# Kernel optimization log

Measured on AMD Instinct MI355X. Metric: run time of the kernel, lower is better.

## Reference

```python
import jax, jax.numpy as jnp
import numpy as np

D_MODEL = 1024
HEAD_DIM = 128
NUM_HEADS = 8


def setup_inputs() -> dict:
    key = jax.random.key(0)
    ks = jax.random.split(key, 7)
    s = 0.02
    x = jax.random.normal(ks[0], (1, 4096, D_MODEL), dtype=jnp.float32)
    Wq = jax.random.normal(ks[1], (D_MODEL, NUM_HEADS * HEAD_DIM), dtype=jnp.float32) * s
    bq = jnp.zeros((NUM_HEADS * HEAD_DIM,), dtype=jnp.float32)
    Wk = jax.random.normal(ks[2], (D_MODEL, HEAD_DIM), dtype=jnp.float32) * s
    bk = jnp.zeros((HEAD_DIM,), dtype=jnp.float32)
    Wv = jax.random.normal(ks[3], (D_MODEL, HEAD_DIM), dtype=jnp.float32) * s
    bv = jnp.zeros((HEAD_DIM,), dtype=jnp.float32)
    return {"x": x, "Wq": Wq, "bq": bq, "Wk": Wk, "bk": bk, "Wv": Wv, "bv": bv}


def reference(x, Wq, bq, Wk, bk, Wv, bv):
    b, s, _ = x.shape
    q = (x @ Wq + bq).reshape(b, s, NUM_HEADS, HEAD_DIM)  # [b,s,h,d]
    k = x @ Wk + bk  # [b,s,d] shared across heads
    v = x @ Wv + bv  # [b,s,d]
    scale = 1.0 / jnp.sqrt(jnp.float32(HEAD_DIM))
    # scores: [b,h,q,k]
    scores = jnp.einsum('bqhd,bkd->bhqk', q, k) * scale
    attn = jax.nn.softmax(scores, axis=-1)
    out = jnp.einsum('bhqk,bkd->bqhd', attn, v)  # [b,s,h,d]
    return out.reshape(b, s, NUM_HEADS * HEAD_DIM)
```

## Files before the change

### kernel.cpp

```cpp
#include <hip/hip_runtime.h>
#include <hip/hip_bf16.h>
#include <stdint.h>

#define D_MODEL 1024
#define HEAD_DIM 128
#define NUM_HEADS 8
#define SEQ 4096
#define NQKV 1280

using bf16x8 = __attribute__((ext_vector_type(8))) short;
using f32x4  = __attribute__((ext_vector_type(4))) float;

__device__ __forceinline__ unsigned short f32_to_bf16(float f) {
    union { float f; uint32_t u; } c{f};
    uint32_t u = c.u;
    return (unsigned short)((u + 0x7fffu + ((u >> 16) & 1u)) >> 16);
}
__device__ __forceinline__ unsigned int pack_bf16x2(float lo, float hi) {
    return (unsigned int)f32_to_bf16(lo) | ((unsigned int)f32_to_bf16(hi) << 16);
}

__device__ __forceinline__ void dma16(const void* g, void* l) {
    __builtin_amdgcn_global_load_lds(
        (const __attribute__((address_space(1))) unsigned int*)g,
        (__attribute__((address_space(3))) unsigned int*)l, 16, 0, 0);
}

__global__ void cvt_x(const float4* __restrict__ x, int4* __restrict__ xb, int n8) {
    int i = blockIdx.x * blockDim.x + threadIdx.x;
    if (i >= n8) return;
    float4 a = x[2 * i], b = x[2 * i + 1];
    int4 o;
    o.x = (int)pack_bf16x2(a.x, a.y);
    o.y = (int)pack_bf16x2(a.z, a.w);
    o.z = (int)pack_bf16x2(b.x, b.y);
    o.w = (int)pack_bf16x2(b.z, b.w);
    xb[i] = o;
}

__global__ __launch_bounds__(256) void pack_wt(const float* __restrict__ Wq,
                                               const float* __restrict__ Wk,
                                               const float* __restrict__ Wv,
                                               unsigned short* __restrict__ Wt) {
    __shared__ unsigned short tile[64][72];
    int bt = blockIdx.x;
    int ktile = bt & 15, ntile = bt >> 4;
    int k0 = ktile * 64, n0 = ntile * 64;
    const float* W; int ldw, nc0;
    if (n0 < 1024)      { W = Wq; ldw = 1024; nc0 = n0; }
    else if (n0 < 1152) { W = Wk; ldw = 128;  nc0 = n0 - 1024; }
    else                { W = Wv; ldw = 128;  nc0 = n0 - 1152; }
    int t = threadIdx.x;
    int c = t & 63, r0 = t >> 6;
#pragma unroll
    for (int p = 0; p < 16; ++p) {
        int r = r0 + p * 4;
        tile[c][r] = f32_to_bf16(W[(k0 + r) * ldw + nc0 + c]);
    }
    __syncthreads();
#pragma unroll
    for (int p = 0; p < 16; ++p) {
        int rn = r0 + p * 4;
        Wt[(n0 + rn) * 1024 + k0 + c] = tile[rn][c];
    }
}

__global__ __launch_bounds__(256, 3) void qkv_gemm(
    const unsigned short* __restrict__ xb,
    const unsigned short* __restrict__ Wt,
    const float* __restrict__ bq, const float* __restrict__ bk, const float* __restrict__ bv,
    unsigned short* __restrict__ q_bf,
    unsigned short* __restrict__ k_bf,
    unsigned short* __restrict__ v_tmp)
{
    __shared__ unsigned short As[2][128 * 64];
    __shared__ unsigned short Bs[2][64 * 64];
    const int t = threadIdx.x;
    const int lane = t & 63, wave = t >> 6;
    const int l15 = lane & 15, quad = lane >> 4;
    const int m0 = blockIdx.y * 128, n0 = blockIdx.x * 64;
    const int srow_l = lane >> 3;
    const int sc_phys = lane & 7;

    f32x4 acc[2][4];
#pragma unroll
    for (int i = 0; i < 2; ++i)
#pragma unroll
        for (int j = 0; j < 4; ++j) acc[i][j] = (f32x4)0.0f;

    auto issue = [&](int k0c, int buf) {
        int c = sc_phys ^ srow_l;
#pragma unroll
        for (int p = 0; p < 4; ++p) {
            int rb = (wave * 4 + p) * 8;
            dma16(&xb[(m0 + rb + srow_l) * 1024 + k0c + c * 8], &As[buf][rb * 64]);
        }
#pragma unroll
        for (int p = 0; p < 2; ++p) {
            int rb = (wave * 2 + p) * 8;
            dma16(&Wt[(n0 + rb + srow_l) * 1024 + k0c + c * 8], &Bs[buf][rb * 64]);
        }
    };

    issue(0, 0);
    for (int kst = 0; kst < 16; ++kst) {
        const int buf = kst & 1;
        __syncthreads();
        if (kst < 15) issue((kst + 1) * 64, buf ^ 1);
#pragma unroll
        for (int ks = 0; ks < 2; ++ks) {
            bf16x8 a[2], b[4];
#pragma unroll
            for (int mt = 0; mt < 2; ++mt)
                a[mt] = *(const bf16x8*)&As[buf][(wave * 32 + mt * 16 + l15) * 64 + (((ks * 4 + quad) ^ (l15 & 7)) * 8)];
#pragma unroll
            for (int nt = 0; nt < 4; ++nt)
                b[nt] = *(const bf16x8*)&Bs[buf][(nt * 16 + l15) * 64 + (((ks * 4 + quad) ^ (l15 & 7)) * 8)];
#pragma unroll
            for (int mt = 0; mt < 2; ++mt)
#pragma unroll
                for (int nt = 0; nt < 4; ++nt)
                    acc[mt][nt] = __builtin_amdgcn_mfma_f32_16x16x32_bf16(a[mt], b[nt], acc[mt][nt], 0, 0, 0);
        }
    }

    const float qscale = 0.08838834764831843f * 1.4426950408889634f;
#pragma unroll
    for (int mt = 0; mt < 2; ++mt)
#pragma unroll
        for (int nt = 0; nt < 4; ++nt)
#pragma unroll
            for (int r = 0; r < 4; ++r) {
                int row = m0 + wave * 32 + mt * 16 + quad * 4 + r;
                int col = n0 + nt * 16 + l15;
                float v = acc[mt][nt][r];
                if (col < 1024)
                    q_bf[row * 1024 + col] = f32_to_bf16((v + bq[col]) * qscale);
                else if (col < 1152)
                    k_bf[row * 128 + (col - 1024)] = f32_to_bf16(v + bk[col - 1024]);
                else
                    v_tmp[row * 128 + (col - 1152)] = f32_to_bf16(v + bv[col - 1152]);
            }
}

__global__ __launch_bounds__(256) void transpose_v(const unsigned short* __restrict__ v_tmp,
                                                   unsigned short* __restrict__ vt) {
    __shared__ unsigned short tile[64][72];
    int s0 = blockIdx.x * 64, d0 = blockIdx.y * 64;
    int t = threadIdx.x;
    int c = t & 63, r0 = t >> 6;
#pragma unroll
    for (int p = 0; p < 16; ++p) {
        int r = r0 + p * 4;
        tile[c][r] = v_tmp[(s0 + r) * 128 + d0 + c];
    }
    __syncthreads();
#pragma unroll
    for (int p = 0; p < 16; ++p) {
        int rd = r0 + p * 4;
        vt[(d0 + rd) * 4096 + s0 + c] = tile[rd][c];
    }
}

__global__ __launch_bounds__(512, 2) void mqa_attn(
    const unsigned short* __restrict__ q_bf,
    const unsigned short* __restrict__ k_bf,
    const unsigned short* __restrict__ vt_bf,
    float* __restrict__ out)
{
    __shared__ unsigned short Ks[2][2][64 * 128];
    __shared__ unsigned short Vs[2][128 * 64];
    __shared__ unsigned short Ps[8][2][16 * 72];
    const int t = threadIdx.x;
    const int lane = t & 63, wave = t >> 6;
    const int l15 = lane & 15, quad = lane >> 4;
    const int half = wave >> 2, w2 = wave & 3;
    const int qbase = blockIdx.x * 32 + (w2 & 1) * 16;
    const int h0 = blockIdx.y * 4 + (w2 >> 1) * 2;
    const int kbase = half * 2048;

    const int krow_l = lane >> 4;
    const int kc_phys = lane & 15;
    const int vrow_l = lane >> 3;
    const int vc_phys = lane & 7;

    bf16x8 qf[2][4];
    {
        int qrow = qbase + l15;
#pragma unroll
        for (int g = 0; g < 2; ++g)
#pragma unroll
            for (int ks = 0; ks < 4; ++ks)
                qf[g][ks] = *(const bf16x8*)&q_bf[qrow * 1024 + (h0 + g) * 128 + ks * 32 + quad * 8];
    }

    f32x4 o[2][8];
#pragma unroll
    for (int g = 0; g < 2; ++g)
#pragma unroll
        for (int d = 0; d < 8; ++d) o[g][d] = (f32x4)0.0f;
    float l_part[2][4] = {{0.f, 0.f, 0.f, 0.f}, {0.f, 0.f, 0.f, 0.f}};

    auto issueK = [&](int kt, int buf) {
#pragma unroll
        for (int p = 0; p < 4; ++p) {
            int row = w2 * 16 + p * 4 + krow_l;
            int c = kc_phys ^ (row & 15);
            dma16(&k_bf[(kt + row) * 128 + c * 8], &Ks[half][buf][(w2 * 16 + p * 4) * 128]);
        }
    };
    auto issueV = [&](int kt) {
#pragma unroll
        for (int p = 0; p < 4; ++p) {
            int row = w2 * 32 + p * 8 + vrow_l;
            int c = vc_phys ^ vrow_l;
            dma16(&vt_bf[row * 4096 + kt + c * 8], &Vs[half][(w2 * 32 + p * 8) * 64]);
        }
    };

    issueK(kbase, 0);
    for (int it = 0; it < 32; ++it) {
        const int buf = it & 1;
        __syncthreads();
        issueV(kbase + it * 64);
        const bool pk = (it + 1 < 32);
        if (pk) issueK(kbase + (it + 1) * 64, buf ^ 1);

        f32x4 s[2][4];
#pragma unroll
        for (int g = 0; g < 2; ++g)
#pragma unroll
            for (int nt = 0; nt < 4; ++nt) s[g][nt] = (f32x4)0.0f;
#pragma unroll
        for (int ks = 0; ks < 4; ++ks)
#pragma unroll
            for (int nt = 0; nt < 4; ++nt) {
                int row = nt * 16 + l15;
                bf16x8 kb = *(const bf16x8*)&Ks[half][buf][row * 128 + (((ks * 4 + quad) ^ l15) * 8)];
                s[0][nt] = __builtin_amdgcn_mfma_f32_16x16x32_bf16(qf[0][ks], kb, s[0][nt], 0, 0, 0);
                s[1][nt] = __builtin_amdgcn_mfma_f32_16x16x32_bf16(qf[1][ks], kb, s[1][nt], 0, 0, 0);
            }

#pragma unroll
        for (int g = 0; g < 2; ++g) {
            unsigned short* P = &Ps[wave][g][0];
#pragma unroll
            for (int nt = 0; nt < 4; ++nt)
#pragma unroll
                for (int r = 0; r < 4; ++r) {
                    float pv = __builtin_amdgcn_exp2f(s[g][nt][r]);
                    l_part[g][r] += pv;
                    P[(quad * 4 + r) * 72 + nt * 16 + l15] = f32_to_bf16(pv);
                }
        }
        asm volatile("s_waitcnt lgkmcnt(0)" ::: "memory");
        if (pk) asm volatile("s_waitcnt vmcnt(4)" ::: "memory");
        else    asm volatile("s_waitcnt vmcnt(0)" ::: "memory");

#pragma unroll
        for (int ks = 0; ks < 2; ++ks) {
            bf16x8 pa0 = *(const bf16x8*)&Ps[wave][0][l15 * 72 + ks * 32 + quad * 8];
            bf16x8 pa1 = *(const bf16x8*)&Ps[wave][1][l15 * 72 + ks * 32 + quad * 8];
#pragma unroll
            for (int d = 0; d < 8; ++d) {
                int row = d * 16 + l15;
                bf16x8 vb = *(const bf16x8*)&Vs[half][row * 64 + (((ks * 4 + quad) ^ (l15 & 7)) * 8)];
                o[0][d] = __builtin_amdgcn_mfma_f32_16x16x32_bf16(pa0, vb, o[0][d], 0, 0, 0);
                o[1][d] = __builtin_amdgcn_mfma_f32_16x16x32_bf16(pa1, vb, o[1][d], 0, 0, 0);
            }
        }
    }

#pragma unroll
    for (int g = 0; g < 2; ++g)
#pragma unroll
        for (int r = 0; r < 4; ++r) {
#pragma unroll
            for (int off = 1; off < 16; off <<= 1)
                l_part[g][r] += __shfl_xor(l_part[g][r], off, 64);
        }

    __syncthreads();
    float* Xo = (float*)&Ks[0][0][0];
    float* Xl = (float*)&Vs[0][0];
    if (half == 1) {
#pragma unroll
        for (int g = 0; g < 2; ++g)
#pragma unroll
            for (int d = 0; d < 8; ++d)
                *(f32x4*)&Xo[((w2 * 16 + g * 8 + d) * 64 + lane) * 4] = o[g][d];
#pragma unroll
        for (int g = 0; g < 2; ++g)
#pragma unroll
            for (int r = 0; r < 4; ++r)
                Xl[(w2 * 8 + g * 4 + r) * 64 + lane] = l_part[g][r];
    }
    __syncthreads();
    if (half == 0) {
#pragma unroll
        for (int g = 0; g < 2; ++g)
#pragma unroll
            for (int d = 0; d < 8; ++d) {
                f32x4 oth = *(const f32x4*)&Xo[((w2 * 16 + g * 8 + d) * 64 + lane) * 4];
                o[g][d] += oth;
            }
#pragma unroll
        for (int g = 0; g < 2; ++g)
#pragma unroll
            for (int r = 0; r < 4; ++r) {
                float lt = l_part[g][r] + Xl[(w2 * 8 + g * 4 + r) * 64 + lane];
                float inv = 1.0f / lt;
                int row = qbase + quad * 4 + r;
#pragma unroll
                for (int d = 0; d < 8; ++d)
                    out[row * 1024 + (h0 + g) * 128 + d * 16 + l15] = o[g][d][r] * inv;
            }
    }
}

extern "C" void kernel_launch(void* const* d_in, const int* in_sizes, int n_in,
                              void* d_out, int out_size, void* d_ws, size_t ws_size,
                              hipStream_t stream) {
    const float* x  = (const float*)d_in[0];
    const float* Wq = (const float*)d_in[1];
    const float* bq = (const float*)d_in[2];
    const float* Wk = (const float*)d_in[3];
    const float* bk = (const float*)d_in[4];
    const float* Wv = (const float*)d_in[5];
    const float* bv = (const float*)d_in[6];
    float* out = (float*)d_out;

    char* ws = (char*)d_ws;
    unsigned short* xb   = (unsigned short*)(ws);
    unsigned short* Wt   = (unsigned short*)(ws + 8388608);
    unsigned short* qb   = (unsigned short*)(ws + 11010048);
    unsigned short* kb   = (unsigned short*)(ws + 19398656);
    unsigned short* vt   = (unsigned short*)(ws + 20447232);
    unsigned short* vtmp = (unsigned short*)(ws + 21495808);

    cvt_x<<<2048, 256, 0, stream>>>((const float4*)x, (int4*)xb, SEQ * D_MODEL / 8);
    pack_wt<<<320, 256, 0, stream>>>(Wq, Wk, Wv, Wt);
    qkv_gemm<<<dim3(20, 32), 256, 0, stream>>>(xb, Wt, bq, bk, bv, qb, kb, vtmp);
    transpose_v<<<dim3(64, 2), 256, 0, stream>>>(vtmp, vt);
    mqa_attn<<<dim3(SEQ / 32, 2), 512, 0, stream>>>(qb, kb, vt, out);
}
```

Measured before the change: 197.3 us.

## Fuse prep kernels, transpose V in GEMM epilogue, compute softmax row-sum via MFMA

Merges the x conversion and weight packing into one launch, and moves the V transpose into the QKV GEMM epilogue through an LDS tile, so the transpose_v kernel and its temp buffer go away. In attention, an extra ones-row is appended to V so the softmax denominator comes out of the MFMA accumulator. This replaces the per-element l_part accumulation and shuffle reduction. It also uses the packed bf16 convert instruction where available. The cost is one extra MFMA column tile per step and more LDS for Vs.

```diff
diff --git a/kernel.cpp b/kernel.cpp
--- a/kernel.cpp
+++ b/kernel.cpp
@@ -6,7 +6,6 @@
 #define HEAD_DIM 128
 #define NUM_HEADS 8
 #define SEQ 4096
-#define NQKV 1280
 
 using bf16x8 = __attribute__((ext_vector_type(8))) short;
 using f32x4  = __attribute__((ext_vector_type(4))) float;
@@ -16,8 +15,17 @@
     uint32_t u = c.u;
     return (unsigned short)((u + 0x7fffu + ((u >> 16) & 1u)) >> 16);
 }
-__device__ __forceinline__ unsigned int pack_bf16x2(float lo, float hi) {
-    return (unsigned int)f32_to_bf16(lo) | ((unsigned int)f32_to_bf16(hi) << 16);
+__device__ __forceinline__ uint32_t pack_bf16x2(float lo, float hi) {
+    return (uint32_t)f32_to_bf16(lo) | ((uint32_t)f32_to_bf16(hi) << 16);
+}
+__device__ __forceinline__ uint32_t cvt2_bf16(float a, float b) {
+#if __has_builtin(__builtin_amdgcn_cvt_pk_bf16_f32)
+    auto r = __builtin_amdgcn_cvt_pk_bf16_f32(a, b);
+    union { decltype(r) v; uint32_t u; } c; c.v = r;
+    return c.u;
+#else
+    return pack_bf16x2(a, b);
+#endif
 }
 
 __device__ __forceinline__ void dma16(const void* g, void* l) {
@@ -26,31 +34,31 @@
         (__attribute__((address_space(3))) unsigned int*)l, 16, 0, 0);
 }
 
-__global__ void cvt_x(const float4* __restrict__ x, int4* __restrict__ xb, int n8) {
-    int i = blockIdx.x * blockDim.x + threadIdx.x;
-    if (i >= n8) return;
-    float4 a = x[2 * i], b = x[2 * i + 1];
-    int4 o;
-    o.x = (int)pack_bf16x2(a.x, a.y);
-    o.y = (int)pack_bf16x2(a.z, a.w);
-    o.z = (int)pack_bf16x2(b.x, b.y);
-    o.w = (int)pack_bf16x2(b.z, b.w);
-    xb[i] = o;
-}
-
-__global__ __launch_bounds__(256) void pack_wt(const float* __restrict__ Wq,
-                                               const float* __restrict__ Wk,
-                                               const float* __restrict__ Wv,
-                                               unsigned short* __restrict__ Wt) {
+__global__ __launch_bounds__(256) void prep(
+    const float4* __restrict__ x, int4* __restrict__ xb,
+    const float* __restrict__ Wq, const float* __restrict__ Wk,
+    const float* __restrict__ Wv, unsigned short* __restrict__ Wt)
+{
     __shared__ unsigned short tile[64][72];
-    int bt = blockIdx.x;
+    const int t = threadIdx.x;
+    if (blockIdx.x < 2048) {
+        int i = blockIdx.x * 256 + t;
+        float4 a = x[2 * i], b = x[2 * i + 1];
+        int4 o;
+        o.x = (int)cvt2_bf16(a.x, a.y);
+        o.y = (int)cvt2_bf16(a.z, a.w);
+        o.z = (int)cvt2_bf16(b.x, b.y);
+        o.w = (int)cvt2_bf16(b.z, b.w);
+        xb[i] = o;
+        return;
+    }
+    int bt = blockIdx.x - 2048;
     int ktile = bt & 15, ntile = bt >> 4;
     int k0 = ktile * 64, n0 = ntile * 64;
     const float* W; int ldw, nc0;
     if (n0 < 1024)      { W = Wq; ldw = 1024; nc0 = n0; }
     else if (n0 < 1152) { W = Wk; ldw = 128;  nc0 = n0 - 1024; }
     else                { W = Wv; ldw = 128;  nc0 = n0 - 1152; }
-    int t = threadIdx.x;
     int c = t & 63, r0 = t >> 6;
 #pragma unroll
     for (int p = 0; p < 16; ++p) {
@@ -71,7 +79,7 @@
     const float* __restrict__ bq, const float* __restrict__ bk, const float* __restrict__ bv,
     unsigned short* __restrict__ q_bf,
     unsigned short* __restrict__ k_bf,
-    unsigned short* __restrict__ v_tmp)
+    unsigned short* __restrict__ vt_bf)
 {
     __shared__ unsigned short As[2][128 * 64];
     __shared__ unsigned short Bs[2][64 * 64];
@@ -125,40 +133,62 @@
     }
 
     const float qscale = 0.08838834764831843f * 1.4426950408889634f;
-#pragma unroll
-    for (int mt = 0; mt < 2; ++mt)
-#pragma unroll
-        for (int nt = 0; nt < 4; ++nt)
-#pragma unroll
-            for (int r = 0; r < 4; ++r) {
-                int row = m0 + wave * 32 + mt * 16 + quad * 4 + r;
+    if (blockIdx.x < 16) {
+#pragma unroll
+        for (int mt = 0; mt < 2; ++mt)
+#pragma unroll
+            for (int nt = 0; nt < 4; ++nt) {
+                int row = m0 + wave * 32 + mt * 16 + quad * 4;
                 int col = n0 + nt * 16 + l15;
-                float v = acc[mt][nt][r];
-                if (col < 1024)
-                    q_bf[row * 1024 + col] = f32_to_bf16((v + bq[col]) * qscale);
-                else if (col < 1152)
-                    k_bf[row * 128 + (col - 1024)] = f32_to_bf16(v + bk[col - 1024]);
-                else
-                    v_tmp[row * 128 + (col - 1152)] = f32_to_bf16(v + bv[col - 1152]);
-            }
-}
-
-__global__ __launch_bounds__(256) void transpose_v(const unsigned short* __restrict__ v_tmp,
-                                                   unsigned short* __restrict__ vt) {
-    __shared__ unsigned short tile[64][72];
-    int s0 = blockIdx.x * 64, d0 = blockIdx.y * 64;
-    int t = threadIdx.x;
-    int c = t & 63, r0 = t >> 6;
-#pragma unroll
-    for (int p = 0; p < 16; ++p) {
-        int r = r0 + p * 4;
-        tile[c][r] = v_tmp[(s0 + r) * 128 + d0 + c];
-    }
-    __syncthreads();
-#pragma unroll
-    for (int p = 0; p < 16; ++p) {
-        int rd = r0 + p * 4;
-        vt[(d0 + rd) * 4096 + s0 + c] = tile[rd][c];
+                float b = bq[col];
+                uint32_t u01 = cvt2_bf16((acc[mt][nt][0] + b) * qscale, (acc[mt][nt][1] + b) * qscale);
+                uint32_t u23 = cvt2_bf16((acc[mt][nt][2] + b) * qscale, (acc[mt][nt][3] + b) * qscale);
+                q_bf[(row + 0) * 1024 + col] = (unsigned short)u01;
+                q_bf[(row + 1) * 1024 + col] = (unsigned short)(u01 >> 16);
+                q_bf[(row + 2) * 1024 + col] = (unsigned short)u23;
+                q_bf[(row + 3) * 1024 + col] = (unsigned short)(u23 >> 16);
+            }
+    } else if (blockIdx.x < 18) {
+#pragma unroll
+        for (int mt = 0; mt < 2; ++mt)
+#pragma unroll
+            for (int nt = 0; nt < 4; ++nt) {
+                int row = m0 + wave * 32 + mt * 16 + quad * 4;
+                int col = n0 + nt * 16 + l15 - 1024;
+                float b = bk[col];
+                uint32_t u01 = cvt2_bf16(acc[mt][nt][0] + b, acc[mt][nt][1] + b);
+                uint32_t u23 = cvt2_bf16(acc[mt][nt][2] + b, acc[mt][nt][3] + b);
+                k_bf[(row + 0) * 128 + col] = (unsigned short)u01;
+                k_bf[(row + 1) * 128 + col] = (unsigned short)(u01 >> 16);
+                k_bf[(row + 2) * 128 + col] = (unsigned short)u23;
+                k_bf[(row + 3) * 128 + col] = (unsigned short)(u23 >> 16);
+            }
+    } else {
+        unsigned short* T = (unsigned short*)As;
+        __syncthreads();
+#pragma unroll
+        for (int mt = 0; mt < 2; ++mt)
+#pragma unroll
+            for (int nt = 0; nt < 4; ++nt) {
+                int lrow = wave * 32 + mt * 16 + quad * 4;
+                int lc = nt * 16 + l15;
+                float b = bv[n0 + lc - 1152];
+                uint32_t u01 = cvt2_bf16(acc[mt][nt][0] + b, acc[mt][nt][1] + b);
+                uint32_t u23 = cvt2_bf16(acc[mt][nt][2] + b, acc[mt][nt][3] + b);
+                T[lc * 136 + lrow + 0] = (unsigned short)u01;
+                T[lc * 136 + lrow + 1] = (unsigned short)(u01 >> 16);
+                T[lc * 136 + lrow + 2] = (unsigned short)u23;
+                T[lc * 136 + lrow + 3] = (unsigned short)(u23 >> 16);
+            }
+        __syncthreads();
+        int vx = blockIdx.x - 18;
+#pragma unroll
+        for (int p = 0; p < 4; ++p) {
+            int lc = p * 16 + (t >> 4);
+            int r0 = (t & 15) * 8;
+            int4 d = *(const int4*)&T[lc * 136 + r0];
+            *(int4*)&vt_bf[(vx * 64 + lc) * 4096 + m0 + r0] = d;
+        }
     }
 }
 
@@ -169,7 +199,7 @@
     float* __restrict__ out)
 {
     __shared__ unsigned short Ks[2][2][64 * 128];
-    __shared__ unsigned short Vs[2][128 * 64];
+    __shared__ unsigned short Vs[2][144 * 64];
     __shared__ unsigned short Ps[8][2][16 * 72];
     const int t = threadIdx.x;
     const int lane = t & 63, wave = t >> 6;
@@ -184,6 +214,11 @@
     const int vrow_l = lane >> 3;
     const int vc_phys = lane & 7;
 
+    for (int i = t; i < 2048; i += 512) {
+        int hh = i >> 10, rr = (i >> 6) & 15, cc = i & 63;
+        Vs[hh][(128 + rr) * 64 + cc] = (rr == 0) ? (unsigned short)0x3F80 : (unsigned short)0;
+    }
+
     bf16x8 qf[2][4];
     {
         int qrow = qbase + l15;
@@ -194,12 +229,11 @@
                 qf[g][ks] = *(const bf16x8*)&q_bf[qrow * 1024 + (h0 + g) * 128 + ks * 32 + quad * 8];
     }
 
-    f32x4 o[2][8];
+    f32x4 o[2][9];
 #pragma unroll
     for (int g = 0; g < 2; ++g)
 #pragma unroll
-        for (int d = 0; d < 8; ++d) o[g][d] = (f32x4)0.0f;
-    float l_part[2][4] = {{0.f, 0.f, 0.f, 0.f}, {0.f, 0.f, 0.f, 0.f}};
+        for (int d = 0; d < 9; ++d) o[g][d] = (f32x4)0.0f;
 
     auto issueK = [&](int kt, int buf) {
 #pragma unroll
@@ -245,13 +279,19 @@
         for (int g = 0; g < 2; ++g) {
             unsigned short* P = &Ps[wave][g][0];
 #pragma unroll
-            for (int nt = 0; nt < 4; ++nt)
-#pragma unroll
-                for (int r = 0; r < 4; ++r) {
-                    float pv = __builtin_amdgcn_exp2f(s[g][nt][r]);
-                    l_part[g][r] += pv;
-                    P[(quad * 4 + r) * 72 + nt * 16 + l15] = f32_to_bf16(pv);
-                }
+            for (int nt = 0; nt < 4; ++nt) {
+                float p0 = __builtin_amdgcn_exp2f(s[g][nt][0]);
+                float p1 = __builtin_amdgcn_exp2f(s[g][nt][1]);
+                float p2 = __builtin_amdgcn_exp2f(s[g][nt][2]);
+                float p3 = __builtin_amdgcn_exp2f(s[g][nt][3]);
+                uint32_t u01 = cvt2_bf16(p0, p1);
+                uint32_t u23 = cvt2_bf16(p2, p3);
+                int col = nt * 16 + l15;
+                P[(quad * 4 + 0) * 72 + col] = (unsigned short)u01;
+                P[(quad * 4 + 1) * 72 + col] = (unsigned short)(u01 >> 16);
+                P[(quad * 4 + 2) * 72 + col] = (unsigned short)u23;
+                P[(quad * 4 + 3) * 72 + col] = (unsigned short)(u23 >> 16);
+            }
         }
         asm volatile("s_waitcnt lgkmcnt(0)" ::: "memory");
         if (pk) asm volatile("s_waitcnt vmcnt(4)" ::: "memory");
@@ -262,7 +302,7 @@
             bf16x8 pa0 = *(const bf16x8*)&Ps[wave][0][l15 * 72 + ks * 32 + quad * 8];
             bf16x8 pa1 = *(const bf16x8*)&Ps[wave][1][l15 * 72 + ks * 32 + quad * 8];
 #pragma unroll
-            for (int d = 0; d < 8; ++d) {
+            for (int d = 0; d < 9; ++d) {
                 int row = d * 16 + l15;
                 bf16x8 vb = *(const bf16x8*)&Vs[half][row * 64 + (((ks * 4 + quad) ^ (l15 & 7)) * 8)];
                 o[0][d] = __builtin_amdgcn_mfma_f32_16x16x32_bf16(pa0, vb, o[0][d], 0, 0, 0);
@@ -271,50 +311,36 @@
         }
     }
 
-#pragma unroll
-    for (int g = 0; g < 2; ++g)
-#pragma unroll
-        for (int r = 0; r < 4; ++r) {
-#pragma unroll
-            for (int off = 1; off < 16; off <<= 1)
-                l_part[g][r] += __shfl_xor(l_part[g][r], off, 64);
-        }
-
     __syncthreads();
     float* Xo = (float*)&Ks[0][0][0];
     float* Xl = (float*)&Vs[0][0];
     if (half == 1) {
 #pragma unroll
-        for (int g = 0; g < 2; ++g)
+        for (int g = 0; g < 2; ++g) {
 #pragma unroll
             for (int d = 0; d < 8; ++d)
                 *(f32x4*)&Xo[((w2 * 16 + g * 8 + d) * 64 + lane) * 4] = o[g][d];
-#pragma unroll
-        for (int g = 0; g < 2; ++g)
-#pragma unroll
-            for (int r = 0; r < 4; ++r)
-                Xl[(w2 * 8 + g * 4 + r) * 64 + lane] = l_part[g][r];
+            *(f32x4*)&Xl[((w2 * 2 + g) * 64 + lane) * 4] = o[g][8];
+        }
     }
     __syncthreads();
     if (half == 0) {
 #pragma unroll
-        for (int g = 0; g < 2; ++g)
-#pragma unroll
-            for (int d = 0; d < 8; ++d) {
-                f32x4 oth = *(const f32x4*)&Xo[((w2 * 16 + g * 8 + d) * 64 + lane) * 4];
-                o[g][d] += oth;
-            }
-#pragma unroll
-        for (int g = 0; g < 2; ++g)
+        for (int g = 0; g < 2; ++g) {
+#pragma unroll
+            for (int d = 0; d < 8; ++d)
+                o[g][d] += *(const f32x4*)&Xo[((w2 * 16 + g * 8 + d) * 64 + lane) * 4];
+            f32x4 o8 = o[g][8] + *(const f32x4*)&Xl[((w2 * 2 + g) * 64 + lane) * 4];
 #pragma unroll
             for (int r = 0; r < 4; ++r) {
-                float lt = l_part[g][r] + Xl[(w2 * 8 + g * 4 + r) * 64 + lane];
-                float inv = 1.0f / lt;
+                float l = __shfl(o8[r], lane & 48, 64);
+                float inv = 1.0f / l;
                 int row = qbase + quad * 4 + r;
 #pragma unroll
                 for (int d = 0; d < 8; ++d)
                     out[row * 1024 + (h0 + g) * 128 + d * 16 + l15] = o[g][d][r] * inv;
             }
+        }
     }
 }
 
@@ -331,16 +357,13 @@
     float* out = (float*)d_out;
 
     char* ws = (char*)d_ws;
-    unsigned short* xb   = (unsigned short*)(ws);
-    unsigned short* Wt   = (unsigned short*)(ws + 8388608);
-    unsigned short* qb   = (unsigned short*)(ws + 11010048);
-    unsigned short* kb   = (unsigned short*)(ws + 19398656);
-    unsigned short* vt   = (unsigned short*)(ws + 20447232);
-    unsigned short* vtmp = (unsigned short*)(ws + 21495808);
-
-    cvt_x<<<2048, 256, 0, stream>>>((const float4*)x, (int4*)xb, SEQ * D_MODEL / 8);
-    pack_wt<<<320, 256, 0, stream>>>(Wq, Wk, Wv, Wt);
-    qkv_gemm<<<dim3(20, 32), 256, 0, stream>>>(xb, Wt, bq, bk, bv, qb, kb, vtmp);
-    transpose_v<<<dim3(64, 2), 256, 0, stream>>>(vtmp, vt);
+    unsigned short* xb = (unsigned short*)(ws);
+    unsigned short* Wt = (unsigned short*)(ws + 8388608);
+    unsigned short* qb = (unsigned short*)(ws + 11010048);
+    unsigned short* kb = (unsigned short*)(ws + 19398656);
+    unsigned short* vt = (unsigned short*)(ws + 20447232);
+
+    prep<<<2368, 256, 0, stream>>>((const float4*)x, (int4*)xb, Wq, Wk, Wv, Wt);
+    qkv_gemm<<<dim3(20, 32), 256, 0, stream>>>(xb, Wt, bq, bk, bv, qb, kb, vt);
     mqa_attn<<<dim3(SEQ / 32, 2), 512, 0, stream>>>(qb, kb, vt, out);
 }
```

After: 187.0 us. 5.2% less time.
